# Kernel tuning notes

Hardware: AMD Instinct MI355X
Metric: run time of the kernel (lower is better)

Reference implementation:

```python
import jax, jax.numpy as jnp
import numpy as np

BSZ, L, H, P = 8, 4096, 512, 256  # batch, seq len, features, complex state dim (conj_sym)
DT_MIN, DT_MAX = 1e-3, 1e-1


def setup_inputs() -> dict:
    key = jax.random.key(0)
    k_u, k_B, k_C, k_D, k_dt = jax.random.split(key, 5)
    u = jax.random.normal(k_u, (BSZ, L, H), dtype=jnp.float32)
    # HiPPO-like stable init for the diagonal state matrix
    Lambda_re = -0.5 * jnp.ones((P,), dtype=jnp.float32)
    Lambda_im = jnp.pi * jnp.arange(P, dtype=jnp.float32)
    # lecun-normal-ish scaling for real/imag parts of B (fan_in = H) and C (fan_in = P)
    B = jax.random.normal(k_B, (P, H, 2), dtype=jnp.float32) / jnp.sqrt(2.0 * H)
    C = jax.random.normal(k_C, (H, P, 2), dtype=jnp.float32) / jnp.sqrt(2.0 * P)
    D = jax.random.normal(k_D, (H,), dtype=jnp.float32)
    log_step = jax.random.uniform(k_dt, (P, 1), dtype=jnp.float32,
                                  minval=jnp.log(DT_MIN), maxval=jnp.log(DT_MAX))
    return {"u": u, "Lambda_re": Lambda_re, "Lambda_im": Lambda_im,
            "B": B, "C": C, "D": D, "log_step": log_step}


def _binop(q_i, q_j):
    """Associative binary operator for diagonal linear recurrence."""
    A_i, b_i = q_i
    A_j, b_j = q_j
    return (A_j * A_i, A_j * b_i + b_j)


def reference(u, Lambda_re, Lambda_im, B, C, D, log_step):
    # --- setup / discretization (zero-order hold) ---
    Lambda = (Lambda_re + 1j * Lambda_im).astype(jnp.complex64)      # (P,)
    B_tilde = (B[..., 0] + 1j * B[..., 1]).astype(jnp.complex64)     # (P,H)
    C_tilde = (C[..., 0] + 1j * C[..., 1]).astype(jnp.complex64)     # (H,P)
    step = jnp.exp(log_step[:, 0])                                   # (P,)
    Lambda_bar = jnp.exp(Lambda * step)                              # (P,)
    B_bar = ((Lambda_bar - 1.0) / Lambda)[:, None] * B_tilde         # (P,H)

    # --- parallel scan over the sequence (diagonal SSM) ---
    Bu = jnp.einsum('blh,ph->blp', u, B_bar)                         # (B,L,P) complex64
    Lam = jnp.broadcast_to(Lambda_bar, Bu.shape)                     # (B,L,P)
    _, xs = jax.lax.associative_scan(_binop, (Lam, Bu), axis=1)      # (B,L,P)

    # --- emissions (factor 2 from conjugate symmetry) + feedthrough ---
    ys = 2.0 * jnp.einsum('blp,hp->blh', xs, C_tilde).real + D * u   # (B,L,H)
    return jax.nn.gelu(ys)
```

## Files before the change

### kernel.cpp

```cpp
#include <hip/hip_runtime.h>
#include <cstdint>
#include <cstddef>

typedef unsigned short u16;
typedef short short8 __attribute__((ext_vector_type(8)));
typedef float floatx4 __attribute__((ext_vector_type(4)));

#define DEVINL __device__ __forceinline__

static constexpr int BSZ = 8, SEQL = 4096, H = 512, P = 256;
static constexpr int M = BSZ * SEQL;
static constexpr int KD = 512;
static constexpr int ND = 512;
static constexpr int CHUNK = 64;
static constexpr int NCH = SEQL / CHUNK;

DEVINL u16 f2bf(float f) {
  union { float f; unsigned u; } v; v.f = f;
  unsigned r = (v.u + 0x7fffu + ((v.u >> 16) & 1u)) >> 16;
  return (u16)r;
}
DEVINL float bf2f(u16 h) {
  union { unsigned u; float f; } v; v.u = ((unsigned)h) << 16; return v.f;
}

DEVINL void gload_lds16(const u16* g, u16* l) {
  __builtin_amdgcn_global_load_lds(
      (const __attribute__((address_space(1))) unsigned*)g,
      (__attribute__((address_space(3))) unsigned*)l, 16, 0, 0);
}

__global__ void setup_kernel(const float* __restrict__ Lre, const float* __restrict__ Lim,
                             const float* __restrict__ logstep,
                             float2* __restrict__ lam, float2* __restrict__ ffac) {
  int p = threadIdx.x;
  if (p >= P) return;
  float lr = Lre[p], li = Lim[p];
  float st = expf(logstep[p]);
  float mag = expf(lr * st);
  float ang = li * st;
  float cr = mag * cosf(ang);
  float ci = mag * sinf(ang);
  lam[p] = make_float2(cr, ci);
  float a = cr - 1.0f, b = ci;
  float den = lr * lr + li * li;
  float fr = (a * lr + b * li) / den;
  float fi = (b * lr - a * li) / den;
  ffac[p] = make_float2(fr, fi);
}

__global__ void bt1_kernel(const float2* __restrict__ Bin,
                           const float2* __restrict__ ffac,
                           u16* __restrict__ bt1) {
  int idx = blockIdx.x * 256 + threadIdx.x;
  int p = idx / H, h = idx % H;
  float2 bv = Bin[(size_t)p * H + h];
  float2 f = ffac[p];
  float br = f.x * bv.x - f.y * bv.y;
  float bi = f.x * bv.y + f.y * bv.x;
  bt1[(size_t)(2 * p) * H + h]     = f2bf(br);
  bt1[(size_t)(2 * p + 1) * H + h] = f2bf(bi);
}

__global__ void bt2_kernel(const float* __restrict__ Cin, u16* __restrict__ bt2) {
  int idx = blockIdx.x * 256 + threadIdx.x;
  float c = Cin[idx];
  float v = (idx & 1) ? -2.0f * c : 2.0f * c;
  bt2[idx] = f2bf(v);
}

__global__ void ucvt_kernel(const float4* __restrict__ uin, ushort4* __restrict__ ubf) {
  int idx = blockIdx.x * 256 + threadIdx.x;
  float4 f = uin[idx];
  ushort4 o;
  o.x = f2bf(f.x); o.y = f2bf(f.y); o.z = f2bf(f.z); o.w = f2bf(f.w);
  ubf[idx] = o;
}

template <int MODE>
__global__ __launch_bounds__(256, 4) void gemm_bt(const u16* __restrict__ A,
                                                  const u16* __restrict__ Bt,
                                                  u16* __restrict__ outBf,
                                                  float* __restrict__ outF,
                                                  const float* __restrict__ Dv,
                                                  const u16* __restrict__ ubf) {
  __shared__ u16 As[2][128 * 32];
  __shared__ u16 Bs[2][128 * 32];
  const int tid = threadIdx.x;
  const int bm = blockIdx.x, bn = blockIdx.y;
  const int wave = tid >> 6, lane = tid & 63;
  const int quad = lane >> 4, l16 = lane & 15;
  const int wm = (wave & 1) << 6, wn = (wave >> 1) << 6;

  floatx4 acc[4][4] = {};

  const u16* Ab = A + (size_t)bm * 128 * KD;
  const u16* Bb = Bt + (size_t)bn * 128 * KD;
  const int srow = tid >> 2;
  const int scol = (tid & 3) << 3;

  gload_lds16(Ab + (size_t)srow * KD + scol,        &As[0][tid * 8]);
  gload_lds16(Ab + (size_t)(srow + 64) * KD + scol, &As[0][2048 + tid * 8]);
  gload_lds16(Bb + (size_t)srow * KD + scol,        &Bs[0][tid * 8]);
  gload_lds16(Bb + (size_t)(srow + 64) * KD + scol, &Bs[0][2048 + tid * 8]);
  asm volatile("s_waitcnt vmcnt(0)" ::: "memory");
  __builtin_amdgcn_sched_barrier(0);
  __builtin_amdgcn_s_barrier();

  int cur = 0;
  for (int k0 = 0; k0 < KD; k0 += 32) {
    if (k0 + 32 < KD) {
      const int nb = cur ^ 1;
      gload_lds16(Ab + (size_t)srow * KD + (k0 + 32) + scol,        &As[nb][tid * 8]);
      gload_lds16(Ab + (size_t)(srow + 64) * KD + (k0 + 32) + scol, &As[nb][2048 + tid * 8]);
      gload_lds16(Bb + (size_t)srow * KD + (k0 + 32) + scol,        &Bs[nb][tid * 8]);
      gload_lds16(Bb + (size_t)(srow + 64) * KD + (k0 + 32) + scol, &Bs[nb][2048 + tid * 8]);
    }

    short8 af[4], bfr[4];
#pragma unroll
    for (int t = 0; t < 4; t++)
      af[t] = *(const short8*)&As[cur][(wm + t * 16 + l16) * 32 + quad * 8];
#pragma unroll
    for (int t = 0; t < 4; t++)
      bfr[t] = *(const short8*)&Bs[cur][(wn + t * 16 + l16) * 32 + quad * 8];

    asm volatile("s_waitcnt lgkmcnt(0)" ::: "memory");
    __builtin_amdgcn_sched_barrier(0);

    __builtin_amdgcn_s_setprio(1);
#pragma unroll
    for (int tm = 0; tm < 4; tm++)
#pragma unroll
      for (int tn = 0; tn < 4; tn++)
        acc[tm][tn] = __builtin_amdgcn_mfma_f32_16x16x32_bf16(af[tm], bfr[tn], acc[tm][tn], 0, 0, 0);
    __builtin_amdgcn_s_setprio(0);

    asm volatile("s_waitcnt vmcnt(0)" ::: "memory");
    __builtin_amdgcn_sched_barrier(0);
    __builtin_amdgcn_s_barrier();
    cur ^= 1;
  }

  const int row_base = bm * 128 + wm + quad * 4;
  const int col_base = bn * 128 + wn + l16;
  float dv[4];
  if (MODE == 1) {
#pragma unroll
    for (int tn = 0; tn < 4; tn++) dv[tn] = Dv[col_base + tn * 16];
  }
#pragma unroll
  for (int tm = 0; tm < 4; tm++) {
#pragma unroll
    for (int tn = 0; tn < 4; tn++) {
      int n = col_base + tn * 16;
#pragma unroll
      for (int r = 0; r < 4; r++) {
        int m = row_base + tm * 16 + r;
        float v = acc[tm][tn][r];
        if (MODE == 0) {
          outBf[(size_t)m * ND + n] = f2bf(v);
        } else {
          float uv = bf2f(ubf[(size_t)m * ND + n]);
          float ys = v + dv[tn] * uv;
          float zz = ys + 0.044715f * (ys * ys * ys);
          float e = __builtin_amdgcn_exp2f(-2.3022082f * zz);
          outF[(size_t)m * ND + n] = ys * __builtin_amdgcn_rcpf(1.0f + e);
        }
      }
    }
  }
}

__global__ __launch_bounds__(256) void scan_carry(const u16* __restrict__ Bu,
                                                  const float2* __restrict__ lam,
                                                  float2* __restrict__ carry) {
  int p = threadIdx.x;
  int c = blockIdx.x;
  int b = blockIdx.y;
  float2 lm = lam[p];
  float xr = 0.f, xi = 0.f;
  const u16* base = Bu + ((size_t)b * SEQL + (size_t)c * CHUNK) * 512 + 2 * p;
  for (int l = 0; l < CHUNK; l++) {
    unsigned w = *(const unsigned*)(base + (size_t)l * 512);
    float br = bf2f((u16)(w & 0xffffu));
    float bi = bf2f((u16)(w >> 16));
    float nr = lm.x * xr - lm.y * xi + br;
    float ni = lm.x * xi + lm.y * xr + bi;
    xr = nr; xi = ni;
  }
  carry[((size_t)b * NCH + c) * P + p] = make_float2(xr, xi);
}

__global__ __launch_bounds__(256) void scan_prefix(const float2* __restrict__ carry,
                                                   const float2* __restrict__ lam,
                                                   float2* __restrict__ prefix) {
  int p = threadIdx.x;
  int b = blockIdx.x;
  float2 lm = lam[p];
  float ar = lm.x, ai = lm.y;
  for (int i = 0; i < 6; i++) { float nr = ar * ar - ai * ai, ni = 2.f * ar * ai; ar = nr; ai = ni; }
  float pr = 0.f, pi = 0.f;
  for (int c = 0; c < NCH; c++) {
    prefix[((size_t)b * NCH + c) * P + p] = make_float2(pr, pi);
    float2 ca = carry[((size_t)b * NCH + c) * P + p];
    float nr = ar * pr - ai * pi + ca.x;
    float ni = ar * pi + ai * pr + ca.y;
    pr = nr; pi = ni;
  }
}

__global__ __launch_bounds__(256) void scan_apply(u16* __restrict__ Bu,
                                                  const float2* __restrict__ lam,
                                                  const float2* __restrict__ prefix) {
  int p = threadIdx.x;
  int c = blockIdx.x;
  int b = blockIdx.y;
  float2 lm = lam[p];
  float2 pf = prefix[((size_t)b * NCH + c) * P + p];
  float xr = pf.x, xi = pf.y;
  u16* base = Bu + ((size_t)b * SEQL + (size_t)c * CHUNK) * 512 + 2 * p;
  for (int l = 0; l < CHUNK; l++) {
    unsigned* addr = (unsigned*)(base + (size_t)l * 512);
    unsigned w = *addr;
    float br = bf2f((u16)(w & 0xffffu));
    float bi = bf2f((u16)(w >> 16));
    float nr = lm.x * xr - lm.y * xi + br;
    float ni = lm.x * xi + lm.y * xr + bi;
    xr = nr; xi = ni;
    *addr = (unsigned)f2bf(nr) | ((unsigned)f2bf(ni) << 16);
  }
}

extern "C" void kernel_launch(void* const* d_in, const int* in_sizes, int n_in,
                              void* d_out, int out_size, void* d_ws, size_t ws_size,
                              hipStream_t stream) {
  const float* u      = (const float*)d_in[0];
  const float* Lre    = (const float*)d_in[1];
  const float* Lim    = (const float*)d_in[2];
  const float* Bin    = (const float*)d_in[3];
  const float* Cin    = (const float*)d_in[4];
  const float* Dv     = (const float*)d_in[5];
  const float* lstep  = (const float*)d_in[6];
  float* out          = (float*)d_out;

  char* ws = (char*)d_ws;
  float2* lam    = (float2*)(ws + 0);
  float2* ffac   = (float2*)(ws + 2048);
  u16*    bt1    = (u16*)   (ws + 4096);
  u16*    bt2    = (u16*)   (ws + 528384);
  u16*    ubf    = (u16*)   (ws + 1052672);
  u16*    Bu     = (u16*)   (ws + 34607104);
  float2* carry  = (float2*)(ws + 68161536);
  float2* prefix = (float2*)(ws + 69210112);

  setup_kernel<<<1, 256, 0, stream>>>(Lre, Lim, lstep, lam, ffac);
  bt1_kernel<<<(P * H) / 256, 256, 0, stream>>>((const float2*)Bin, ffac, bt1);
  bt2_kernel<<<(H * P * 2) / 256, 256, 0, stream>>>(Cin, bt2);
  ucvt_kernel<<<(M * H / 4) / 256, 256, 0, stream>>>((const float4*)u, (ushort4*)ubf);

  gemm_bt<0><<<dim3(M / 128, ND / 128), 256, 0, stream>>>(ubf, bt1, Bu, nullptr, nullptr, nullptr);

  scan_carry <<<dim3(NCH, BSZ), 256, 0, stream>>>(Bu, lam, carry);
  scan_prefix<<<BSZ, 256, 0, stream>>>(carry, lam, prefix);
  scan_apply <<<dim3(NCH, BSZ), 256, 0, stream>>>(Bu, lam, prefix);

  gemm_bt<1><<<dim3(M / 128, ND / 128), 256, 0, stream>>>(Bu, bt2, nullptr, out, Dv, ubf);
}
```

Baseline: 204.0 us.

## Triple-buffer GEMM LDS staging and remap blocks across XCDs

The GEMM main loop goes from double to triple buffering in LDS, prefetching two k-steps ahead and waiting only on the older loads (vmcnt(4)), with the loop fully unrolled. The 2D grid is flattened to 1D and block IDs are remapped so that consecutive hardware blocks, which are dispatched round-robin across the 8 XCDs, land on neighbouring tiles within one XCD for better L2 reuse. The goal is to hide more global-load latency and improve cache locality. In exchange, LDS use per block rises and launch bounds drop to 3 blocks per CU, lowering occupancy.

```diff
diff --git a/kernel.cpp b/kernel.cpp
--- a/kernel.cpp
+++ b/kernel.cpp
@@ -78,16 +78,21 @@
 }
 
 template <int MODE>
-__global__ __launch_bounds__(256, 4) void gemm_bt(const u16* __restrict__ A,
+__global__ __launch_bounds__(256, 3) void gemm_bt(const u16* __restrict__ A,
                                                   const u16* __restrict__ Bt,
                                                   u16* __restrict__ outBf,
                                                   float* __restrict__ outF,
                                                   const float* __restrict__ Dv,
                                                   const u16* __restrict__ ubf) {
-  __shared__ u16 As[2][128 * 32];
-  __shared__ u16 Bs[2][128 * 32];
+  __shared__ u16 As[3][128 * 32];
+  __shared__ u16 Bs[3][128 * 32];
   const int tid = threadIdx.x;
-  const int bm = blockIdx.x, bn = blockIdx.y;
+
+  const int hw = blockIdx.x;
+  const int logical = (hw & 7) * 128 + (hw >> 3);
+  const int bm = logical >> 2;
+  const int bn = logical & 3;
+
   const int wave = tid >> 6, lane = tid & 63;
   const int quad = lane >> 4, l16 = lane & 15;
   const int wm = (wave & 1) << 6, wn = (wave >> 1) << 6;
@@ -99,23 +104,28 @@
   const int srow = tid >> 2;
   const int scol = (tid & 3) << 3;
 
-  gload_lds16(Ab + (size_t)srow * KD + scol,        &As[0][tid * 8]);
-  gload_lds16(Ab + (size_t)(srow + 64) * KD + scol, &As[0][2048 + tid * 8]);
-  gload_lds16(Bb + (size_t)srow * KD + scol,        &Bs[0][tid * 8]);
-  gload_lds16(Bb + (size_t)(srow + 64) * KD + scol, &Bs[0][2048 + tid * 8]);
-  asm volatile("s_waitcnt vmcnt(0)" ::: "memory");
+#define STAGE(buf, kofs)                                                            \
+  do {                                                                              \
+    gload_lds16(Ab + (size_t)srow * KD + (kofs) + scol,        &As[buf][tid * 8]);  \
+    gload_lds16(Ab + (size_t)(srow + 64) * KD + (kofs) + scol, &As[buf][2048 + tid * 8]); \
+    gload_lds16(Bb + (size_t)srow * KD + (kofs) + scol,        &Bs[buf][tid * 8]);  \
+    gload_lds16(Bb + (size_t)(srow + 64) * KD + (kofs) + scol, &Bs[buf][2048 + tid * 8]); \
+  } while (0)
+
+  STAGE(0, 0);
+  STAGE(1, 32);
+  asm volatile("s_waitcnt vmcnt(4)" ::: "memory");
   __builtin_amdgcn_sched_barrier(0);
   __builtin_amdgcn_s_barrier();
-
-  int cur = 0;
-  for (int k0 = 0; k0 < KD; k0 += 32) {
-    if (k0 + 32 < KD) {
-      const int nb = cur ^ 1;
-      gload_lds16(Ab + (size_t)srow * KD + (k0 + 32) + scol,        &As[nb][tid * 8]);
-      gload_lds16(Ab + (size_t)(srow + 64) * KD + (k0 + 32) + scol, &As[nb][2048 + tid * 8]);
-      gload_lds16(Bb + (size_t)srow * KD + (k0 + 32) + scol,        &Bs[nb][tid * 8]);
-      gload_lds16(Bb + (size_t)(srow + 64) * KD + (k0 + 32) + scol, &Bs[nb][2048 + tid * 8]);
-    }
+  __builtin_amdgcn_sched_barrier(0);
+
+  constexpr int NK = KD / 32;
+#pragma unroll
+  for (int ks = 0; ks < NK; ks++) {
+    const int k0 = ks * 32;
+    const int cur = ks % 3;
+
+    if (ks + 2 < NK) STAGE((ks + 2) % 3, k0 + 64);
 
     short8 af[4], bfr[4];
 #pragma unroll
@@ -136,11 +146,19 @@
         acc[tm][tn] = __builtin_amdgcn_mfma_f32_16x16x32_bf16(af[tm], bfr[tn], acc[tm][tn], 0, 0, 0);
     __builtin_amdgcn_s_setprio(0);
 
-    asm volatile("s_waitcnt vmcnt(0)" ::: "memory");
-    __builtin_amdgcn_sched_barrier(0);
-    __builtin_amdgcn_s_barrier();
-    cur ^= 1;
-  }
+    if (ks + 2 < NK) {
+      asm volatile("s_waitcnt vmcnt(4)" ::: "memory");
+      __builtin_amdgcn_sched_barrier(0);
+      __builtin_amdgcn_s_barrier();
+      __builtin_amdgcn_sched_barrier(0);
+    } else if (ks + 1 < NK) {
+      asm volatile("s_waitcnt vmcnt(0)" ::: "memory");
+      __builtin_amdgcn_sched_barrier(0);
+      __builtin_amdgcn_s_barrier();
+      __builtin_amdgcn_sched_barrier(0);
+    }
+  }
+#undef STAGE
 
   const int row_base = bm * 128 + wm + quad * 4;
   const int col_base = bn * 128 + wn + l16;
@@ -259,11 +277,11 @@
   bt2_kernel<<<(H * P * 2) / 256, 256, 0, stream>>>(Cin, bt2);
   ucvt_kernel<<<(M * H / 4) / 256, 256, 0, stream>>>((const float4*)u, (ushort4*)ubf);
 
-  gemm_bt<0><<<dim3(M / 128, ND / 128), 256, 0, stream>>>(ubf, bt1, Bu, nullptr, nullptr, nullptr);
+  gemm_bt<0><<<M / 128 * (ND / 128), 256, 0, stream>>>(ubf, bt1, Bu, nullptr, nullptr, nullptr);
 
   scan_carry <<<dim3(NCH, BSZ), 256, 0, stream>>>(Bu, lam, carry);
   scan_prefix<<<BSZ, 256, 0, stream>>>(carry, lam, prefix);
   scan_apply <<<dim3(NCH, BSZ), 256, 0, stream>>>(Bu, lam, prefix);
 
-  gemm_bt<1><<<dim3(M / 128, ND / 128), 256, 0, stream>>>(Bu, bt2, nullptr, out, Dv, ubf);
-}
+  gemm_bt<1><<<M / 128 * (ND / 128), 256, 0, stream>>>(Bu, bt2, nullptr, out, Dv, ubf);
+}
```

New measurement: 205.5 us. No clear change (+0.7%).
